# Optimization experiments

Measured on AMD Instinct MI355X. Metric: run time of the kernel, lower is better.

The kernel has to match this reference:

```python
import jax, jax.numpy as jnp
import numpy as np

B, T, D, H = 16, 1024, 768, 64

def setup_inputs() -> dict:
    key = jax.random.key(0)
    k1, k2, k3, k4 = jax.random.split(key, 4)
    scale = 0.02
    x = jax.random.normal(k1, (B, T, D), dtype=jnp.float32)
    Wq = jax.random.normal(k2, (H, D), dtype=jnp.float32) * scale
    Wk = jax.random.normal(k3, (H, D), dtype=jnp.float32) * scale
    Wv = jax.random.normal(k4, (H, D), dtype=jnp.float32) * scale
    return {"x": x, "Wq": Wq, "Wk": Wk, "Wv": Wv}

def reference(x, Wq, Wk, Wv):
    # q,k,v: [B,T,H]  (nn.Linear with no bias: x @ W^T)
    q = jnp.einsum('btd,hd->bth', x, Wq)
    k = jnp.einsum('btd,hd->bth', x, Wk)
    v = jnp.einsum('btd,hd->bth', x, Wv)
    T_ = x.shape[1]
    # NOTE: original scales by emb_dim**-0.5 (not head_size**-0.5)
    scores = jnp.einsum('bth,bsh->bts', q, k) * (x.shape[-1] ** -0.5)
    causal = jnp.tril(jnp.ones((T_, T_), dtype=bool))
    scores = jnp.where(causal, scores, -jnp.inf)
    attn = jax.nn.softmax(scores, axis=-1)
    return jnp.einsum('bts,bsh->bth', attn, v)
```

## Files before the change

kernel.cpp:

```cpp
#include <hip/hip_runtime.h>
#include <hip/hip_bf16.h>

typedef __attribute__((ext_vector_type(8))) short bf16x8;
typedef __attribute__((ext_vector_type(4))) float f32x4;

#define BATCH 16
#define SEQ   1024
#define EMB   768
#define HEAD  64
#define NT    (BATCH*SEQ)
#define NQKV  192

__device__ inline ushort f2bf(float f) {
  __hip_bfloat16 h = __float2bfloat16(f);
  return *reinterpret_cast<const ushort*>(&h);
}

__device__ inline void lds_dma16(const void* g, void* l) {
  __builtin_amdgcn_global_load_lds(
      (const __attribute__((address_space(1))) void*)g,
      (__attribute__((address_space(3))) void*)l, 16, 0, 0);
}

__global__ __launch_bounds__(256) void convw_kernel(
    const float* __restrict__ Wq, const float* __restrict__ Wk,
    const float* __restrict__ Wv, ushort* __restrict__ wt)
{
  const int row = blockIdx.x * 8 + (threadIdx.x >> 5);
  const float* W = (row < 64) ? Wq : (row < 128 ? Wk : Wv);
  const int r = row & 63;
  #pragma unroll
  for (int j = 0; j < 3; ++j) {
    const int c = (threadIdx.x & 31) + 32 * j;
    const int grp = c >> 3, gst = c & 7;
    const int glog = gst ^ (row & 7);
    const int srccol = (grp << 6) + (glog << 3);
    const float4 f0 = *reinterpret_cast<const float4*>(&W[(size_t)r * EMB + srccol]);
    const float4 f1 = *reinterpret_cast<const float4*>(&W[(size_t)r * EMB + srccol + 4]);
    union { ushort us[8]; uint4 u; } o;
    o.us[0]=f2bf(f0.x); o.us[1]=f2bf(f0.y); o.us[2]=f2bf(f0.z); o.us[3]=f2bf(f0.w);
    o.us[4]=f2bf(f1.x); o.us[5]=f2bf(f1.y); o.us[6]=f2bf(f1.z); o.us[7]=f2bf(f1.w);
    *reinterpret_cast<uint4*>(&wt[(size_t)row * EMB + (c << 3)]) = o.u;
  }
}

__global__ __launch_bounds__(512, 4) void proj_kernel(
    const float* __restrict__ x, const ushort* __restrict__ wt,
    ushort* __restrict__ qo, ushort* __restrict__ ko, ushort* __restrict__ vo)
{
  __shared__ ushort Xl[2][64 * 64];
  __shared__ ushort Wl[2][192 * 64];

  const int tid  = threadIdx.x;
  const int wave = tid >> 6, lane = tid & 63;
  const int m0   = blockIdx.x * 64;
  const int wr   = wave >> 2, wc = wave & 3;
  const int col16 = lane & 15, quad = lane >> 4;

  const int xrow = tid >> 3;
  const int xc   = (tid & 7) * 8;
  const int xchk = tid & 7;

  float4 xa, xb;

  #define LOADX(kt_) {                                                          \
    xa = *reinterpret_cast<const float4*>(&x[(size_t)(m0 + xrow) * EMB + (kt_) * 64 + xc]);     \
    xb = *reinterpret_cast<const float4*>(&x[(size_t)(m0 + xrow) * EMB + (kt_) * 64 + xc + 4]); }

  #define WRITEX(buf_) {                                                        \
    union { ushort us[8]; uint4 u; } p;                                         \
    p.us[0]=f2bf(xa.x); p.us[1]=f2bf(xa.y); p.us[2]=f2bf(xa.z); p.us[3]=f2bf(xa.w); \
    p.us[4]=f2bf(xb.x); p.us[5]=f2bf(xb.y); p.us[6]=f2bf(xb.z); p.us[7]=f2bf(xb.w); \
    *reinterpret_cast<uint4*>(&Xl[buf_][xrow * 64 + ((xchk ^ (xrow & 7)) << 3)]) = p.u; }

  #define STAGEW(kt_, buf_) { _Pragma("unroll")                                 \
    for (int u = 0; u < 3; ++u) {                                               \
      lds_dma16(&wt[(size_t)(u * 64 + (tid >> 3)) * EMB + (kt_) * 64 + (tid & 7) * 8], \
                &Wl[buf_][(u * 64 + wave * 8) * 64]);                           \
    } }

  f32x4 acc[2][3];
  #pragma unroll
  for (int m = 0; m < 2; ++m)
    #pragma unroll
    for (int n = 0; n < 3; ++n) acc[m][n] = (f32x4){0.f, 0.f, 0.f, 0.f};

  LOADX(0); STAGEW(0, 0); WRITEX(0);

  int cur = 0;
  for (int kt = 0; kt < 12; ++kt) {
    __syncthreads();
    if (kt < 11) { LOADX(kt + 1); STAGEW(kt + 1, cur ^ 1); }
    #pragma unroll
    for (int ks = 0; ks < 2; ++ks) {
      const int g = ks * 4 + quad;
      bf16x8 a[2];
      #pragma unroll
      for (int m = 0; m < 2; ++m) {
        const int ar = wr * 32 + 16 * m + col16;
        a[m] = *reinterpret_cast<const bf16x8*>(&Xl[cur][ar * 64 + ((g ^ (ar & 7)) << 3)]);
      }
      #pragma unroll
      for (int n = 0; n < 3; ++n) {
        const int br = wc * 48 + 16 * n + col16;
        const bf16x8 b = *reinterpret_cast<const bf16x8*>(&Wl[cur][br * 64 + ((g ^ (br & 7)) << 3)]);
        #pragma unroll
        for (int m = 0; m < 2; ++m)
          acc[m][n] = __builtin_amdgcn_mfma_f32_16x16x32_bf16(a[m], b, acc[m][n], 0, 0, 0);
      }
    }
    if (kt < 11) WRITEX(cur ^ 1);
    cur ^= 1;
  }

  #pragma unroll
  for (int n = 0; n < 3; ++n) {
    const int c   = wc * 48 + 16 * n + col16;
    const int sel = c >> 6, h = c & 63;
    #pragma unroll
    for (int m = 0; m < 2; ++m) {
      #pragma unroll
      for (int i = 0; i < 4; ++i) {
        const int t = m0 + wr * 32 + 16 * m + quad * 4 + i;
        const ushort val = f2bf(acc[m][n][i]);
        if (sel == 0) {
          qo[(size_t)t * HEAD + h] = val;
        } else if (sel == 1) {
          const int hs = (((h >> 3) ^ (t & 7)) << 3) | (h & 7);
          ko[(size_t)t * HEAD + hs] = val;
        } else {
          const int bb = t >> 10, tin = t & 1023;
          const int ts = (tin & ~63) | (((((tin >> 3) & 7) ^ (h & 7))) << 3) | (tin & 7);
          vo[((size_t)bb * HEAD + h) * SEQ + ts] = val;
        }
      }
    }
  }
  #undef LOADX
  #undef WRITEX
  #undef STAGEW
}

__global__ __launch_bounds__(256) void attn_kernel(
    const ushort* __restrict__ q, const ushort* __restrict__ k,
    const ushort* __restrict__ vT, float* __restrict__ out,
    float* __restrict__ po, float* __restrict__ pl)
{
  __shared__ ushort Kl[2][64 * 64];
  __shared__ ushort Vl[2][64 * 64];
  __shared__ ushort lp[4][16][72];

  const int tid  = threadIdx.x;
  const int wave = tid >> 6, lane = tid & 63;
  const int bid  = blockIdx.x;
  const int b    = bid & 15;
  const int u    = bid >> 4;

  int j, s, ns;
  if (u < 4)       { j = u;                s = 0;           ns = 1; }
  else if (u < 12) { j = 4 + ((u - 4) >> 1);  s = (u - 4) & 1; ns = 2; }
  else             { j = 8 + ((u - 12) >> 2); s = (u - 12) & 3; ns = 4; }

  const int qt0 = j * 64;
  const int nt  = j + 1;
  const int t0  = (nt * s) / ns;
  const int t1  = (nt * (s + 1)) / ns;
  const float SC2 = 0.03608439182435161f * 1.4426950408889634f;

  const int col  = lane & 15;
  const int quad = lane >> 4;
  const int koff = quad * 8;

  const size_t qb = ((size_t)b * SEQ + qt0 + 16 * wave + col) * HEAD;
  const bf16x8 qa0 = *reinterpret_cast<const bf16x8*>(&q[qb + koff]);
  const bf16x8 qa1 = *reinterpret_cast<const bf16x8*>(&q[qb + koff + 32]);

  #define STAGE(t_, buf_) {                                                     \
    _Pragma("unroll")                                                           \
    for (int r = 0; r < 2; ++r)                                                 \
      lds_dma16(&k[((size_t)b * SEQ + (t_) * 64 + r * 32 + wave * 8 + (lane >> 3)) * HEAD + (lane & 7) * 8], \
                &Kl[buf_][(r * 32 + wave * 8) * 64]);                           \
    _Pragma("unroll")                                                           \
    for (int r = 0; r < 2; ++r)                                                 \
      lds_dma16(&vT[((size_t)b * HEAD + r * 32 + wave * 8 + (lane >> 3)) * SEQ + (t_) * 64 + (lane & 7) * 8], \
                &Vl[buf_][(r * 32 + wave * 8) * 64]);                           \
  }

  f32x4 o[4];
  #pragma unroll
  for (int hf = 0; hf < 4; ++hf) o[hf] = (f32x4){0.f, 0.f, 0.f, 0.f};
  float l_part[4];
  #pragma unroll
  for (int i = 0; i < 4; ++i) l_part[i] = 0.f;

  STAGE(t0, 0);

  for (int t = t0; t < t1; ++t) {
    const int cur = (t - t0) & 1;
    __syncthreads();
    if (t + 1 < t1) STAGE(t + 1, cur ^ 1);

    f32x4 sreg[4];
    #pragma unroll
    for (int f = 0; f < 4; ++f) {
      const int rowf = 16 * f + col;
      const bf16x8 kb0 = *reinterpret_cast<const bf16x8*>(
          &Kl[cur][rowf * 64 + ((quad ^ (rowf & 7)) << 3)]);
      const bf16x8 kb1 = *reinterpret_cast<const bf16x8*>(
          &Kl[cur][rowf * 64 + (((quad + 4) ^ (rowf & 7)) << 3)]);
      f32x4 z = (f32x4){0.f, 0.f, 0.f, 0.f};
      z       = __builtin_amdgcn_mfma_f32_16x16x32_bf16(qa0, kb0, z, 0, 0, 0);
      sreg[f] = __builtin_amdgcn_mfma_f32_16x16x32_bf16(qa1, kb1, z, 0, 0, 0);
    }

    const bool last = (t == nt - 1);
    #pragma unroll
    for (int f = 0; f < 4; ++f) {
      const int kvc = t * 64 + 16 * f + col;
      #pragma unroll
      for (int i = 0; i < 4; ++i) {
        float v = sreg[f][i];
        if (last && kvc > qt0 + 16 * wave + quad * 4 + i) v = -1e30f;
        const float p = exp2f(v * SC2);
        l_part[i] += p;
        lp[wave][quad * 4 + i][16 * f + col] = f2bf(p);
      }
    }

    #pragma unroll
    for (int ks = 0; ks < 2; ++ks) {
      const bf16x8 pa = *reinterpret_cast<const bf16x8*>(&lp[wave][col][ks * 32 + koff]);
      #pragma unroll
      for (int hf = 0; hf < 4; ++hf) {
        const int vrow = 16 * hf + col;
        const int g = ks * 4 + quad;
        const bf16x8 vb = *reinterpret_cast<const bf16x8*>(
            &Vl[cur][vrow * 64 + ((g ^ (vrow & 7)) << 3)]);
        o[hf] = __builtin_amdgcn_mfma_f32_16x16x32_bf16(pa, vb, o[hf], 0, 0, 0);
      }
    }
  }

  #pragma unroll
  for (int i = 0; i < 4; ++i) {
    #pragma unroll
    for (int d = 1; d < 16; d <<= 1) l_part[i] += __shfl_xor(l_part[i], d);
  }

  if (ns == 1) {
    #pragma unroll
    for (int i = 0; i < 4; ++i) {
      const float inv = 1.0f / l_part[i];
      const int tq = qt0 + 16 * wave + quad * 4 + i;
      #pragma unroll
      for (int hf = 0; hf < 4; ++hf)
        out[((size_t)b * SEQ + tq) * HEAD + 16 * hf + col] = o[hf][i] * inv;
    }
  } else {
    const int su = u - 4;
    const int pidx = b * 40 + su;
    float* pob = &po[(size_t)pidx * 4096];
    #pragma unroll
    for (int i = 0; i < 4; ++i) {
      const int r = 16 * wave + quad * 4 + i;
      #pragma unroll
      for (int hf = 0; hf < 4; ++hf)
        pob[r * 64 + 16 * hf + col] = o[hf][i];
      if (col == 0) pl[pidx * 64 + r] = l_part[i];
    }
  }
  #undef STAGE
}

__global__ __launch_bounds__(256) void combine_kernel(
    const float* __restrict__ po, const float* __restrict__ pl,
    float* __restrict__ out)
{
  const int idx = blockIdx.x * 256 + threadIdx.x;
  const int c = idx & 63;
  const int r = (idx >> 6) & 63;
  const int e = idx >> 12;
  const int jj = e % 12, b = e / 12;
  const int j = 4 + jj;
  const int su0 = (j < 8) ? (j - 4) * 2 : 8 + (j - 8) * 4;
  const int ns  = (j < 8) ? 2 : 4;
  float num = 0.f, den = 0.f;
  for (int s = 0; s < ns; ++s) {
    const int pidx = b * 40 + su0 + s;
    num += po[(size_t)pidx * 4096 + r * 64 + c];
    den += pl[pidx * 64 + r];
  }
  out[((size_t)b * SEQ + j * 64 + r) * HEAD + c] = num / den;
}

extern "C" void kernel_launch(void* const* d_in, const int* in_sizes, int n_in,
                              void* d_out, int out_size, void* d_ws, size_t ws_size,
                              hipStream_t stream) {
  const float* x  = (const float*)d_in[0];
  const float* Wq = (const float*)d_in[1];
  const float* Wk = (const float*)d_in[2];
  const float* Wv = (const float*)d_in[3];

  char* base = (char*)d_ws;
  ushort* qw  = (ushort*)(base);
  ushort* kw  = (ushort*)(base + (2u << 20));
  ushort* vTw = (ushort*)(base + (4u << 20));
  ushort* wtw = (ushort*)(base + (6u << 20));
  float*  po  = (float*) (base + (8u << 20));
  float*  pl  = (float*) (base + (20u << 20));
  float*  out = (float*)d_out;

  convw_kernel<<<NQKV / 8, 256, 0, stream>>>(Wq, Wk, Wv, wtw);
  proj_kernel<<<NT / 64, 512, 0, stream>>>(x, wtw, qw, kw, vTw);
  attn_kernel<<<BATCH * 44, 256, 0, stream>>>(qw, kw, vTw, out, po, pl);
  combine_kernel<<<786432 / 256, 256, 0, stream>>>(po, pl, out);
}
```

Measured before the change: 44.16 us.

## Split projection tiles into 32-row by 96-column blocks of 256 threads

```diff
diff --git a/kernel.cpp b/kernel.cpp
--- a/kernel.cpp
+++ b/kernel.cpp
@@ -44,28 +44,29 @@
   }
 }
 
-__global__ __launch_bounds__(512, 4) void proj_kernel(
+__global__ __launch_bounds__(256) void proj_kernel(
     const float* __restrict__ x, const ushort* __restrict__ wt,
     ushort* __restrict__ qo, ushort* __restrict__ ko, ushort* __restrict__ vo)
 {
-  __shared__ ushort Xl[2][64 * 64];
-  __shared__ ushort Wl[2][192 * 64];
+  __shared__ ushort Xl[2][32 * 64];
+  __shared__ ushort Wl[2][96 * 64];
 
   const int tid  = threadIdx.x;
   const int wave = tid >> 6, lane = tid & 63;
-  const int m0   = blockIdx.x * 64;
-  const int wr   = wave >> 2, wc = wave & 3;
+  const int m0   = (blockIdx.x >> 1) * 32;
+  const int nb96 = (blockIdx.x & 1) * 96;
+  const int wr   = wave >> 1, wc = wave & 1;
   const int col16 = lane & 15, quad = lane >> 4;
 
   const int xrow = tid >> 3;
-  const int xc   = (tid & 7) * 8;
   const int xchk = tid & 7;
 
   float4 xa, xb;
 
   #define LOADX(kt_) {                                                          \
-    xa = *reinterpret_cast<const float4*>(&x[(size_t)(m0 + xrow) * EMB + (kt_) * 64 + xc]);     \
-    xb = *reinterpret_cast<const float4*>(&x[(size_t)(m0 + xrow) * EMB + (kt_) * 64 + xc + 4]); }
+    const float* p = &x[(size_t)(m0 + xrow) * EMB + (kt_) * 64 + xchk * 8];     \
+    xa = *reinterpret_cast<const float4*>(p);                                   \
+    xb = *reinterpret_cast<const float4*>(p + 4); }
 
   #define WRITEX(buf_) {                                                        \
     union { ushort us[8]; uint4 u; } p;                                         \
@@ -75,15 +76,13 @@
 
   #define STAGEW(kt_, buf_) { _Pragma("unroll")                                 \
     for (int u = 0; u < 3; ++u) {                                               \
-      lds_dma16(&wt[(size_t)(u * 64 + (tid >> 3)) * EMB + (kt_) * 64 + (tid & 7) * 8], \
-                &Wl[buf_][(u * 64 + wave * 8) * 64]);                           \
+      lds_dma16(&wt[(size_t)(nb96 + u * 32 + wave * 8 + (lane >> 3)) * EMB + (kt_) * 64 + (lane & 7) * 8], \
+                &Wl[buf_][(u * 32 + wave * 8) * 64]);                           \
     } }
 
-  f32x4 acc[2][3];
-  #pragma unroll
-  for (int m = 0; m < 2; ++m)
-    #pragma unroll
-    for (int n = 0; n < 3; ++n) acc[m][n] = (f32x4){0.f, 0.f, 0.f, 0.f};
+  f32x4 acc[3];
+  #pragma unroll
+  for (int n = 0; n < 3; ++n) acc[n] = (f32x4){0.f, 0.f, 0.f, 0.f};
 
   LOADX(0); STAGEW(0, 0); WRITEX(0);
 
@@ -94,19 +93,15 @@
     #pragma unroll
     for (int ks = 0; ks < 2; ++ks) {
       const int g = ks * 4 + quad;
-      bf16x8 a[2];
-      #pragma unroll
-      for (int m = 0; m < 2; ++m) {
-        const int ar = wr * 32 + 16 * m + col16;
-        a[m] = *reinterpret_cast<const bf16x8*>(&Xl[cur][ar * 64 + ((g ^ (ar & 7)) << 3)]);
-      }
+      const int ar = wr * 16 + col16;
+      const bf16x8 a = *reinterpret_cast<const bf16x8*>(
+          &Xl[cur][ar * 64 + ((g ^ (ar & 7)) << 3)]);
       #pragma unroll
       for (int n = 0; n < 3; ++n) {
         const int br = wc * 48 + 16 * n + col16;
-        const bf16x8 b = *reinterpret_cast<const bf16x8*>(&Wl[cur][br * 64 + ((g ^ (br & 7)) << 3)]);
-        #pragma unroll
-        for (int m = 0; m < 2; ++m)
-          acc[m][n] = __builtin_amdgcn_mfma_f32_16x16x32_bf16(a[m], b, acc[m][n], 0, 0, 0);
+        const bf16x8 b = *reinterpret_cast<const bf16x8*>(
+            &Wl[cur][br * 64 + ((g ^ (br & 7)) << 3)]);
+        acc[n] = __builtin_amdgcn_mfma_f32_16x16x32_bf16(a, b, acc[n], 0, 0, 0);
       }
     }
     if (kt < 11) WRITEX(cur ^ 1);
@@ -115,24 +110,21 @@
 
   #pragma unroll
   for (int n = 0; n < 3; ++n) {
-    const int c   = wc * 48 + 16 * n + col16;
+    const int c   = nb96 + wc * 48 + 16 * n + col16;
     const int sel = c >> 6, h = c & 63;
     #pragma unroll
-    for (int m = 0; m < 2; ++m) {
-      #pragma unroll
-      for (int i = 0; i < 4; ++i) {
-        const int t = m0 + wr * 32 + 16 * m + quad * 4 + i;
-        const ushort val = f2bf(acc[m][n][i]);
-        if (sel == 0) {
-          qo[(size_t)t * HEAD + h] = val;
-        } else if (sel == 1) {
-          const int hs = (((h >> 3) ^ (t & 7)) << 3) | (h & 7);
-          ko[(size_t)t * HEAD + hs] = val;
-        } else {
-          const int bb = t >> 10, tin = t & 1023;
-          const int ts = (tin & ~63) | (((((tin >> 3) & 7) ^ (h & 7))) << 3) | (tin & 7);
-          vo[((size_t)bb * HEAD + h) * SEQ + ts] = val;
-        }
+    for (int i = 0; i < 4; ++i) {
+      const int t = m0 + wr * 16 + quad * 4 + i;
+      const ushort val = f2bf(acc[n][i]);
+      if (sel == 0) {
+        qo[(size_t)t * HEAD + h] = val;
+      } else if (sel == 1) {
+        const int hs = (((h >> 3) ^ (t & 7)) << 3) | (h & 7);
+        ko[(size_t)t * HEAD + hs] = val;
+      } else {
+        const int bb = t >> 10, tin = t & 1023;
+        const int ts = (tin & ~63) | (((((tin >> 3) & 7) ^ (h & 7))) << 3) | (tin & 7);
+        vo[((size_t)bb * HEAD + h) * SEQ + ts] = val;
       }
     }
   }
@@ -311,7 +303,7 @@
   float*  out = (float*)d_out;
 
   convw_kernel<<<NQKV / 8, 256, 0, stream>>>(Wq, Wk, Wv, wtw);
-  proj_kernel<<<NT / 64, 512, 0, stream>>>(x, wtw, qw, kw, vTw);
+  proj_kernel<<<(NT / 32) * 2, 256, 0, stream>>>(x, wtw, qw, kw, vTw);
   attn_kernel<<<BATCH * 44, 256, 0, stream>>>(qw, kw, vTw, out, po, pl);
   combine_kernel<<<786432 / 256, 256, 0, stream>>>(po, pl, out);
 }
```

New measurement: 46.17 us. 4.5% more time.
